# Optimization experiments

Hardware: AMD Instinct MI355X
Metric: run time of the kernel (lower is better)

## Reference

```python
import jax, jax.numpy as jnp
import numpy as np

# (dv=3, dc=6)-regular Tanner graph: M checks, N=2M vars, E=M*dc edges
M, N, DV, DC, D, B, T = 1024, 2048, 3, 6, 8, 128, 5
CIN = DC * D          # check-MLP in/out dim = 48
VIN = DV * D + 1      # var-MLP in/out dim  = 25 (extra scalar = LLR)
HC, HV = 4 * CIN, 4 * VIN
EPS = 1e-6


def _graph():
    # variable j connects to checks (j + l) % M, l = 0..DV-1 -> every check has degree DC
    var_nbrs = (np.arange(N)[:, None] + np.arange(DV)[None, :]) % M   # [N, DV] check ids
    # var-edge id e = j*DV + l ; sort edges by check to get check-slot ordering
    order = np.argsort(var_nbrs.reshape(-1), kind='stable')           # check-edge p -> var-edge e
    chk_nbrs = (order // DV).reshape(M, DC)                           # var id in each check slot
    inv_order = np.argsort(order)                                     # var-edge e -> check-edge p
    return chk_nbrs, order, inv_order


def setup_inputs() -> dict:
    key = jax.random.key(0)
    ks = jax.random.split(key, 12)
    chk_nbrs, order, inv_order = _graph()
    prior = np.clip(np.random.default_rng(0).uniform(0.005, 0.05, size=N), EPS, 1 - EPS)
    prior_llr = jnp.asarray(np.log((1.0 - prior) / prior), jnp.float32)

    def lin_w(k, g, nin, nout):
        return jax.random.normal(k, (g, nin, nout), jnp.float32) / np.sqrt(nin)

    def lin_b(k, g, nout):
        return 0.02 * jax.random.normal(k, (g, nout), jnp.float32)

    return {
        "syndromes": jax.random.randint(ks[0], (B, M), 0, 2, jnp.int32),
        "prior_llr": prior_llr,
        "chk_w1": lin_w(ks[1], M, CIN, HC), "chk_b1": lin_b(ks[2], M, HC),
        "chk_w2": lin_w(ks[3], M, HC, CIN), "chk_b2": lin_b(ks[4], M, CIN),
        "var_w1": lin_w(ks[5], N, VIN, HV), "var_b1": lin_b(ks[6], N, HV),
        "var_w2": lin_w(ks[7], N, HV, VIN), "var_b2": lin_b(ks[8], N, VIN),
        "chk_nbrs": jnp.asarray(chk_nbrs, jnp.int32),      # [M, DC] var id per check slot
        "c2v_gather": jnp.asarray(inv_order, jnp.int32),   # var-edge -> check-edge perm
        "v2c_gather": jnp.asarray(order, jnp.int32),       # check-edge -> var-edge perm
    }


def reference(syndromes, prior_llr, chk_w1, chk_b1, chk_w2, chk_b2,
              var_w1, var_b1, var_w2, var_b2, chk_nbrs, c2v_gather, v2c_gather):
    synd_sgn = (1 - 2 * syndromes).astype(jnp.float32)                    # [B, M]
    prior_b = jnp.broadcast_to(prior_llr, (B, N))[..., None]              # [B, N, 1]

    def chk_mlp(x):  # x: [B, M, CIN], per-check grouped GEMM
        h = jax.nn.gelu(jnp.einsum('bmi,mih->bmh', x, chk_w1) + chk_b1, approximate=False)
        return jnp.einsum('bmh,mho->bmo', h, chk_w2) + chk_b2

    def var_mlp(x):  # x: [B, N, VIN]
        h = jax.nn.gelu(jnp.einsum('bni,nih->bnh', x, var_w1) + var_b1, approximate=False)
        return jnp.einsum('bnh,nho->bno', h, var_w2) + var_b2

    # init check in-messages: zeros with first component = prior LLR of neighbor var
    chk_in = jnp.zeros((B, M, DC, D), jnp.float32).at[..., 0].set(prior_llr[chk_nbrs][None])

    def step(chk_in, _):
        y = chk_mlp(chk_in.reshape(B, M, CIN)).reshape(B, M, DC, D)
        y = y * synd_sgn[:, :, None, None]                                # syndrome sign flip
        var_in = y.reshape(B, M * DC, D)[:, c2v_gather]                   # scatter c->v as gather
        x = jnp.concatenate([var_in.reshape(B, N, DV * D), prior_b], axis=-1)
        out = var_mlp(x)
        llr = out[..., DV * D]                                            # [B, N]
        msg = out[..., :DV * D].reshape(B, N * DV, D)
        chk_in_new = msg[:, v2c_gather].reshape(B, M, DC, D)              # scatter v->c as gather
        return chk_in_new, llr

    _, llrs = jax.lax.scan(step, chk_in, None, length=T)
    return llrs  # [T, B, N]
```

## Files before the change

kernel.cpp:

```cpp
#include <hip/hip_runtime.h>
#include <math.h>

#define MM 1024
#define NN 2048
#define BB 128
#define TT 5
#define EE 6144

typedef __bf16 bf16x8 __attribute__((ext_vector_type(8)));
typedef float  f32x4  __attribute__((ext_vector_type(4)));
typedef unsigned int u32x4 __attribute__((ext_vector_type(4)));

__device__ __forceinline__ float gelu_fast(float x) {
    float xe = x * 0.70710678118654752f;
    float ax = fabsf(xe);
    float t  = __builtin_amdgcn_rcpf(1.0f + 0.3275911f * ax);
    float p  = t * (0.254829592f + t * (-0.284496736f + t * (1.421413741f +
               t * (-1.453152027f + t * 1.061405429f))));
    float er = 1.0f - p * __expf(-xe * xe);
    er = copysignf(er, xe);
    return 0.5f * x * (1.0f + er);
}

__device__ __forceinline__ void wave_lds_fence() {
    asm volatile("s_waitcnt lgkmcnt(0)" ::: "memory");
}

__global__ __launch_bounds__(256)
void init_kernel(const float* __restrict__ prior, __bf16* __restrict__ v2c)
{
    int idx = blockIdx.x * 256 + threadIdx.x;
    int e = idx >> 7;
    bf16x8 v;
    #pragma unroll
    for (int j = 0; j < 8; ++j) v[j] = (__bf16)0.0f;
    v[0] = (__bf16)prior[e / 3];
    *(bf16x8*)(v2c + (size_t)idx * 8) = v;
}

__global__ __launch_bounds__(256)
void prep_chk(const float* __restrict__ w1g, const float* __restrict__ w2g,
              __bf16* __restrict__ wchk)
{
    const int m = blockIdx.x;
    const int tid = threadIdx.x, w = tid >> 6, l = tid & 63, qq = l >> 4, cc = l & 15;
    const float* s1 = w1g + (size_t)m * (48 * 192);
    const float* s2 = w2g + (size_t)m * (192 * 48);
    __bf16* dst = wchk + (size_t)m * 21504;
    for (int f = w; f < 42; f += 4) {
        bf16x8 v;
        if (f < 24) {
            int kt = f / 12, nt = f % 12;
            #pragma unroll
            for (int j = 0; j < 8; ++j) {
                int k = kt * 32 + qq * 8 + j, n = nt * 16 + cc;
                v[j] = (k < 48) ? (__bf16)s1[k * 192 + n] : (__bf16)0.0f;
            }
        } else {
            int g = f - 24, kt = g / 3, nt = g % 3;
            #pragma unroll
            for (int j = 0; j < 8; ++j) {
                int k = kt * 32 + qq * 8 + j, n = nt * 16 + cc;
                v[j] = (__bf16)s2[k * 48 + n];
            }
        }
        *(bf16x8*)(dst + f * 512 + l * 8) = v;
    }
}

__global__ __launch_bounds__(256)
void prep_var(const float* __restrict__ w1g, const float* __restrict__ w2g,
              __bf16* __restrict__ wvar)
{
    const int nv = blockIdx.x;
    const int tid = threadIdx.x, w = tid >> 6, l = tid & 63, qq = l >> 4, cc = l & 15;
    const float* s1 = w1g + (size_t)nv * (25 * 100);
    const float* s2 = w2g + (size_t)nv * (100 * 25);
    __bf16* dst = wvar + (size_t)nv * 7680;
    for (int f = w; f < 15; f += 4) {
        bf16x8 v;
        if (f < 7) {
            int nt = f;
            #pragma unroll
            for (int j = 0; j < 8; ++j) {
                int k = qq * 8 + j, n = nt * 16 + cc;
                v[j] = (k < 25 && n < 100) ? (__bf16)s1[k * 100 + n] : (__bf16)0.0f;
            }
        } else {
            int g = f - 7, kt = g >> 1, nt = g & 1;
            #pragma unroll
            for (int j = 0; j < 8; ++j) {
                int k = kt * 32 + qq * 8 + j, n = nt * 16 + cc;
                v[j] = (k < 100 && n < 25) ? (__bf16)s2[k * 25 + n] : (__bf16)0.0f;
            }
        }
        *(bf16x8*)(dst + f * 512 + l * 8) = v;
    }
}

__global__ __launch_bounds__(256, 2)
void chk_kernel(const __bf16* __restrict__ wchk,
                const float* __restrict__ b1g, const float* __restrict__ b2g,
                const int* __restrict__ syndromes,
                const int* __restrict__ v2c_gather,
                const __bf16* __restrict__ v2c, __bf16* __restrict__ c2v)
{
    const int m = blockIdx.x;
    const int tid = threadIdx.x;
    const int w = tid >> 6, l = tid & 63, q = l >> 4, c = l & 15;

    __shared__ __align__(16) __bf16 wAll[42 * 512];
    __shared__ __align__(16) __bf16 hb[4 * 3200];
    __shared__ float b1s[192];
    __shared__ float b2s[48];
    __shared__ float sgns[128];
    __shared__ int   eg[6];

    {
        const __bf16* wsrc = wchk + (size_t)m * 21504;
        for (int f = w; f < 42; f += 4) {
            u32x4 v = *(const u32x4*)(wsrc + f * 512 + l * 8);
            *(u32x4*)(wAll + f * 512 + l * 8) = v;
        }
    }
    if (tid < 192) b1s[tid] = b1g[(size_t)m * 192 + tid];
    if (tid < 48)  b2s[tid] = b2g[(size_t)m * 48 + tid];
    if (tid < 128) sgns[tid] = (float)(1 - 2 * syndromes[(size_t)tid * MM + m]);
    if (tid < 6)   eg[tid] = v2c_gather[m * 6 + tid];
    __syncthreads();

    const __bf16* w1f = wAll;
    const __bf16* w2f = wAll + 24 * 512;
    __bf16* myh = hb + w * 3200;
    const int e0 = eg[q];
    const int e1 = (q < 2) ? eg[4 + q] : 0;

    for (int t2 = 0; t2 < 2; ++t2) {
        const int bt = t2 * 64 + w * 16;

        bf16x8 a0 = *(const bf16x8*)(v2c + ((size_t)e0 * BB + bt + c) * 8);
        bf16x8 a1;
        #pragma unroll
        for (int j = 0; j < 8; ++j) a1[j] = (__bf16)0.0f;
        if (q < 2) a1 = *(const bf16x8*)(v2c + ((size_t)e1 * BB + bt + c) * 8);

        f32x4 acc[12];
        #pragma unroll
        for (int nt = 0; nt < 12; ++nt) {
            bf16x8 bf0 = *(const bf16x8*)(w1f + (nt * 64 + l) * 8);
            bf16x8 bf1 = *(const bf16x8*)(w1f + ((12 + nt) * 64 + l) * 8);
            f32x4 z = {0.f, 0.f, 0.f, 0.f};
            z = __builtin_amdgcn_mfma_f32_16x16x32_bf16(a0, bf0, z, 0, 0, 0);
            z = __builtin_amdgcn_mfma_f32_16x16x32_bf16(a1, bf1, z, 0, 0, 0);
            acc[nt] = z;
        }

        #pragma unroll
        for (int nt = 0; nt < 12; ++nt) {
            #pragma unroll
            for (int r = 0; r < 4; ++r) {
                int row = q * 4 + r, col = nt * 16 + c;
                float h = acc[nt][r] + b1s[col];
                myh[row * 200 + col] = (__bf16)gelu_fast(h);
            }
        }
        wave_lds_fence();

        f32x4 acc2[3];
        #pragma unroll
        for (int nt = 0; nt < 3; ++nt) acc2[nt] = (f32x4){0.f, 0.f, 0.f, 0.f};
        #pragma unroll
        for (int kt = 0; kt < 6; ++kt) {
            bf16x8 a = *(const bf16x8*)(myh + c * 200 + kt * 32 + q * 8);
            #pragma unroll
            for (int nt = 0; nt < 3; ++nt) {
                bf16x8 bfr = *(const bf16x8*)(w2f + ((kt * 3 + nt) * 64 + l) * 8);
                acc2[nt] = __builtin_amdgcn_mfma_f32_16x16x32_bf16(a, bfr, acc2[nt], 0, 0, 0);
            }
        }
        wave_lds_fence();

        #pragma unroll
        for (int nt = 0; nt < 3; ++nt) {
            #pragma unroll
            for (int r = 0; r < 4; ++r) {
                int row = q * 4 + r, col = nt * 16 + c;
                float yv = (acc2[nt][r] + b2s[col]) * sgns[bt + row];
                myh[row * 72 + col] = (__bf16)yv;
            }
        }
        wave_lds_fence();

        {
            int s = l >> 4, row = l & 15;
            u32x4 vv = *(const u32x4*)(myh + row * 72 + s * 8);
            *(u32x4*)(c2v + ((size_t)(m * 6 + s) * BB + bt + row) * 8) = vv;
            if (l < 32) {
                int s2 = (64 + l) >> 4, row2 = l & 15;
                u32x4 v2 = *(const u32x4*)(myh + row2 * 72 + s2 * 8);
                *(u32x4*)(c2v + ((size_t)(m * 6 + s2) * BB + bt + row2) * 8) = v2;
            }
        }
        wave_lds_fence();
    }
}

__global__ __launch_bounds__(256, 4)
void var_kernel(const __bf16* __restrict__ wvar,
                const float* __restrict__ b1g, const float* __restrict__ b2g,
                const int* __restrict__ c2v_gather, const float* __restrict__ prior,
                const __bf16* __restrict__ c2v, __bf16* __restrict__ v2c,
                float* __restrict__ llr_out)
{
    const int nv = blockIdx.x;
    const int tid = threadIdx.x;
    const int w = tid >> 6, l = tid & 63, q = l >> 4, c = l & 15;

    __shared__ __align__(16) __bf16 wAll[15 * 512];
    __shared__ __align__(16) __bf16 hb[4 * 2816];
    __shared__ float b1s[112];
    __shared__ float b2s[32];
    __shared__ int   cgs[3];

    {
        u32x4* zp = (u32x4*)hb;
        for (int i = tid; i < 1408; i += 256) zp[i] = (u32x4){0, 0, 0, 0};
    }
    {
        const __bf16* wsrc = wvar + (size_t)nv * 7680;
        for (int f = w; f < 15; f += 4) {
            u32x4 v = *(const u32x4*)(wsrc + f * 512 + l * 8);
            *(u32x4*)(wAll + f * 512 + l * 8) = v;
        }
    }
    if (tid < 112) b1s[tid] = (tid < 100) ? b1g[(size_t)nv * 100 + tid] : 0.0f;
    if (tid < 32)  b2s[tid] = (tid < 25) ? b2g[(size_t)nv * 25 + tid] : 0.0f;
    if (tid < 3)   cgs[tid] = c2v_gather[nv * 3 + tid];
    __syncthreads();

    const __bf16* w1vf = wAll;
    const __bf16* w2vf = wAll + 7 * 512;
    __bf16* myh = hb + w * 2816;
    __bf16* myy = hb + w * 2816 + 2176;
    const float pr = prior[nv];
    const __bf16 prbf = (__bf16)pr;
    const int ep = (q < 3) ? cgs[q] : 0;

    for (int t2 = 0; t2 < 2; ++t2) {
        const int bt = t2 * 64 + w * 16;

        bf16x8 a;
        #pragma unroll
        for (int j = 0; j < 8; ++j) a[j] = (__bf16)0.0f;
        if (q < 3) {
            a = *(const bf16x8*)(c2v + ((size_t)ep * BB + bt + c) * 8);
        } else {
            a[0] = prbf;
        }

        f32x4 acc[7];
        #pragma unroll
        for (int nt = 0; nt < 7; ++nt) {
            bf16x8 bfr = *(const bf16x8*)(w1vf + (nt * 64 + l) * 8);
            f32x4 z = {0.f, 0.f, 0.f, 0.f};
            acc[nt] = __builtin_amdgcn_mfma_f32_16x16x32_bf16(a, bfr, z, 0, 0, 0);
        }

        #pragma unroll
        for (int nt = 0; nt < 7; ++nt) {
            #pragma unroll
            for (int r = 0; r < 4; ++r) {
                int row = q * 4 + r, col = nt * 16 + c;
                float h = acc[nt][r] + b1s[col];
                myh[row * 136 + col] = (__bf16)gelu_fast(h);
            }
        }
        wave_lds_fence();

        f32x4 acc2[2];
        acc2[0] = (f32x4){0.f, 0.f, 0.f, 0.f};
        acc2[1] = (f32x4){0.f, 0.f, 0.f, 0.f};
        #pragma unroll
        for (int kt = 0; kt < 4; ++kt) {
            bf16x8 a2 = *(const bf16x8*)(myh + c * 136 + kt * 32 + q * 8);
            #pragma unroll
            for (int nt = 0; nt < 2; ++nt) {
                bf16x8 bfr = *(const bf16x8*)(w2vf + ((kt * 2 + nt) * 64 + l) * 8);
                acc2[nt] = __builtin_amdgcn_mfma_f32_16x16x32_bf16(a2, bfr, acc2[nt], 0, 0, 0);
            }
        }
        wave_lds_fence();

        #pragma unroll
        for (int nt = 0; nt < 2; ++nt) {
            #pragma unroll
            for (int r = 0; r < 4; ++r) {
                int row = q * 4 + r, col = nt * 16 + c;
                float yv = acc2[nt][r] + b2s[col];
                if (col < 24) myy[row * 40 + col] = (__bf16)yv;
                else if (col == 24) llr_out[(size_t)(bt + row) * NN + nv] = yv;
            }
        }
        wave_lds_fence();

        if (l < 48) {
            int s = l >> 4, row = l & 15;
            u32x4 vv = *(const u32x4*)(myy + row * 40 + s * 8);
            *(u32x4*)(v2c + ((size_t)(nv * 3 + s) * BB + bt + row) * 8) = vv;
        }
        wave_lds_fence();
    }
}

extern "C" void kernel_launch(void* const* d_in, const int* in_sizes, int n_in,
                              void* d_out, int out_size, void* d_ws, size_t ws_size,
                              hipStream_t stream) {
    const int*   syndromes = (const int*)  d_in[0];
    const float* prior_llr = (const float*)d_in[1];
    const float* chk_w1    = (const float*)d_in[2];
    const float* chk_b1    = (const float*)d_in[3];
    const float* chk_w2    = (const float*)d_in[4];
    const float* chk_b2    = (const float*)d_in[5];
    const float* var_w1    = (const float*)d_in[6];
    const float* var_b1    = (const float*)d_in[7];
    const float* var_w2    = (const float*)d_in[8];
    const float* var_b2    = (const float*)d_in[9];
    const int*   c2v_g     = (const int*)  d_in[11];
    const int*   v2c_g     = (const int*)  d_in[12];

    float* out = (float*)d_out;

    __bf16* v2c  = (__bf16*)d_ws;
    __bf16* c2v  = v2c + (size_t)EE * BB * 8;
    __bf16* wchk = c2v + (size_t)EE * BB * 8;
    __bf16* wvar = wchk + (size_t)MM * 21504;

    prep_chk<<<MM, 256, 0, stream>>>(chk_w1, chk_w2, wchk);
    prep_var<<<NN, 256, 0, stream>>>(var_w1, var_w2, wvar);
    init_kernel<<<EE * BB / 256, 256, 0, stream>>>(prior_llr, v2c);

    for (int t = 0; t < TT; ++t) {
        chk_kernel<<<MM, 256, 0, stream>>>(wchk, chk_b1, chk_b2,
                                           syndromes, v2c_g, v2c, c2v);
        var_kernel<<<NN, 256, 0, stream>>>(wvar, var_b1, var_b2,
                                           c2v_g, prior_llr, c2v, v2c,
                                           out + (size_t)t * BB * NN);
    }
}
```

Before: 475.2 us.

## Read MLP weights directly from global memory, merge prep kernels, skip final message write

The check and var kernels no longer stage per-node weights, biases, signs and gather indices through LDS behind a block barrier. Each wave now reads the MFMA weight fragments straight from global memory and keeps biases and syndrome signs in registers, which cuts LDS use and lets chk_kernel target 4 blocks per SM. The two weight-prep kernels are merged into one launch with one wave per fragment, and the last var pass skips writing v2c messages that are never read. In exchange, all four waves of a block re-read the same weights from global memory or cache instead of sharing an LDS copy.

```diff
diff --git a/kernel.cpp b/kernel.cpp
--- a/kernel.cpp
+++ b/kernel.cpp
@@ -10,6 +10,7 @@
 typedef __bf16 bf16x8 __attribute__((ext_vector_type(8)));
 typedef float  f32x4  __attribute__((ext_vector_type(4)));
 typedef unsigned int u32x4 __attribute__((ext_vector_type(4)));
+typedef unsigned int u32x2 __attribute__((ext_vector_type(2)));
 
 __device__ __forceinline__ float gelu_fast(float x) {
     float xe = x * 0.70710678118654752f;
@@ -39,66 +40,59 @@
 }
 
 __global__ __launch_bounds__(256)
-void prep_chk(const float* __restrict__ w1g, const float* __restrict__ w2g,
-              __bf16* __restrict__ wchk)
+void prep_all(const float* __restrict__ cw1, const float* __restrict__ cw2,
+              const float* __restrict__ vw1, const float* __restrict__ vw2,
+              __bf16* __restrict__ wchk, __bf16* __restrict__ wvar)
 {
-    const int m = blockIdx.x;
-    const int tid = threadIdx.x, w = tid >> 6, l = tid & 63, qq = l >> 4, cc = l & 15;
-    const float* s1 = w1g + (size_t)m * (48 * 192);
-    const float* s2 = w2g + (size_t)m * (192 * 48);
-    __bf16* dst = wchk + (size_t)m * 21504;
-    for (int f = w; f < 42; f += 4) {
-        bf16x8 v;
+    const int wid = blockIdx.x * 4 + (threadIdx.x >> 6);
+    const int l = threadIdx.x & 63, qq = l >> 4, cc = l & 15;
+    bf16x8 v;
+    __bf16* dst;
+    if (wid < MM * 42) {
+        const int m = wid / 42, f = wid % 42;
         if (f < 24) {
-            int kt = f / 12, nt = f % 12;
+            const int kt = f / 12, nt = f % 12;
+            const float* s1 = cw1 + (size_t)m * (48 * 192);
             #pragma unroll
             for (int j = 0; j < 8; ++j) {
-                int k = kt * 32 + qq * 8 + j, n = nt * 16 + cc;
-                v[j] = (k < 48) ? (__bf16)s1[k * 192 + n] : (__bf16)0.0f;
+                int k = kt * 32 + qq * 8 + j;
+                v[j] = (k < 48) ? (__bf16)s1[k * 192 + nt * 16 + cc] : (__bf16)0.0f;
             }
         } else {
-            int g = f - 24, kt = g / 3, nt = g % 3;
+            const int g = f - 24, kt = g / 3, nt = g % 3;
+            const float* s2 = cw2 + (size_t)m * (192 * 48);
             #pragma unroll
             for (int j = 0; j < 8; ++j) {
-                int k = kt * 32 + qq * 8 + j, n = nt * 16 + cc;
-                v[j] = (__bf16)s2[k * 48 + n];
-            }
-        }
-        *(bf16x8*)(dst + f * 512 + l * 8) = v;
-    }
-}
-
-__global__ __launch_bounds__(256)
-void prep_var(const float* __restrict__ w1g, const float* __restrict__ w2g,
-              __bf16* __restrict__ wvar)
-{
-    const int nv = blockIdx.x;
-    const int tid = threadIdx.x, w = tid >> 6, l = tid & 63, qq = l >> 4, cc = l & 15;
-    const float* s1 = w1g + (size_t)nv * (25 * 100);
-    const float* s2 = w2g + (size_t)nv * (100 * 25);
-    __bf16* dst = wvar + (size_t)nv * 7680;
-    for (int f = w; f < 15; f += 4) {
-        bf16x8 v;
+                int k = kt * 32 + qq * 8 + j;
+                v[j] = (__bf16)s2[k * 48 + nt * 16 + cc];
+            }
+        }
+        dst = wchk + (size_t)m * 21504 + (f * 64 + l) * 8;
+    } else {
+        const int tsk = wid - MM * 42;
+        const int nv = tsk / 15, f = tsk % 15;
         if (f < 7) {
-            int nt = f;
+            const float* s1 = vw1 + (size_t)nv * (25 * 100);
             #pragma unroll
             for (int j = 0; j < 8; ++j) {
-                int k = qq * 8 + j, n = nt * 16 + cc;
+                int k = qq * 8 + j, n = f * 16 + cc;
                 v[j] = (k < 25 && n < 100) ? (__bf16)s1[k * 100 + n] : (__bf16)0.0f;
             }
         } else {
-            int g = f - 7, kt = g >> 1, nt = g & 1;
+            const int g = f - 7, kt = g >> 1, nt = g & 1;
+            const float* s2 = vw2 + (size_t)nv * (100 * 25);
             #pragma unroll
             for (int j = 0; j < 8; ++j) {
                 int k = kt * 32 + qq * 8 + j, n = nt * 16 + cc;
                 v[j] = (k < 100 && n < 25) ? (__bf16)s2[k * 25 + n] : (__bf16)0.0f;
             }
         }
-        *(bf16x8*)(dst + f * 512 + l * 8) = v;
-    }
-}
-
-__global__ __launch_bounds__(256, 2)
+        dst = wvar + (size_t)nv * 7680 + (f * 64 + l) * 8;
+    }
+    *(bf16x8*)dst = v;
+}
+
+__global__ __launch_bounds__(256, 4)
 void chk_kernel(const __bf16* __restrict__ wchk,
                 const float* __restrict__ b1g, const float* __restrict__ b2g,
                 const int* __restrict__ syndromes,
@@ -109,31 +103,26 @@
     const int tid = threadIdx.x;
     const int w = tid >> 6, l = tid & 63, q = l >> 4, c = l & 15;
 
-    __shared__ __align__(16) __bf16 wAll[42 * 512];
     __shared__ __align__(16) __bf16 hb[4 * 3200];
-    __shared__ float b1s[192];
-    __shared__ float b2s[48];
-    __shared__ float sgns[128];
-    __shared__ int   eg[6];
-
-    {
-        const __bf16* wsrc = wchk + (size_t)m * 21504;
-        for (int f = w; f < 42; f += 4) {
-            u32x4 v = *(const u32x4*)(wsrc + f * 512 + l * 8);
-            *(u32x4*)(wAll + f * 512 + l * 8) = v;
-        }
-    }
-    if (tid < 192) b1s[tid] = b1g[(size_t)m * 192 + tid];
-    if (tid < 48)  b2s[tid] = b2g[(size_t)m * 48 + tid];
-    if (tid < 128) sgns[tid] = (float)(1 - 2 * syndromes[(size_t)tid * MM + m]);
-    if (tid < 6)   eg[tid] = v2c_gather[m * 6 + tid];
-    __syncthreads();
-
-    const __bf16* w1f = wAll;
-    const __bf16* w2f = wAll + 24 * 512;
     __bf16* myh = hb + w * 3200;
-    const int e0 = eg[q];
-    const int e1 = (q < 2) ? eg[4 + q] : 0;
+
+    const __bf16* wb = wchk + (size_t)m * 21504;
+
+    float b1v[12], b2v[3], sg[8];
+    #pragma unroll
+    for (int nt = 0; nt < 12; ++nt) b1v[nt] = b1g[(size_t)m * 192 + nt * 16 + c];
+    #pragma unroll
+    for (int nt = 0; nt < 3; ++nt)  b2v[nt] = b2g[(size_t)m * 48 + nt * 16 + c];
+    #pragma unroll
+    for (int t2 = 0; t2 < 2; ++t2)
+        #pragma unroll
+        for (int r = 0; r < 4; ++r) {
+            int row = t2 * 64 + w * 16 + q * 4 + r;
+            sg[t2 * 4 + r] = (float)(1 - 2 * syndromes[(size_t)row * MM + m]);
+        }
+
+    const int e0 = v2c_gather[m * 6 + q];
+    const int e1 = (q < 2) ? v2c_gather[m * 6 + 4 + q] : 0;
 
     for (int t2 = 0; t2 < 2; ++t2) {
         const int bt = t2 * 64 + w * 16;
@@ -147,8 +136,8 @@
         f32x4 acc[12];
         #pragma unroll
         for (int nt = 0; nt < 12; ++nt) {
-            bf16x8 bf0 = *(const bf16x8*)(w1f + (nt * 64 + l) * 8);
-            bf16x8 bf1 = *(const bf16x8*)(w1f + ((12 + nt) * 64 + l) * 8);
+            bf16x8 bf0 = *(const bf16x8*)(wb + (nt * 64 + l) * 8);
+            bf16x8 bf1 = *(const bf16x8*)(wb + ((12 + nt) * 64 + l) * 8);
             f32x4 z = {0.f, 0.f, 0.f, 0.f};
             z = __builtin_amdgcn_mfma_f32_16x16x32_bf16(a0, bf0, z, 0, 0, 0);
             z = __builtin_amdgcn_mfma_f32_16x16x32_bf16(a1, bf1, z, 0, 0, 0);
@@ -159,9 +148,8 @@
         for (int nt = 0; nt < 12; ++nt) {
             #pragma unroll
             for (int r = 0; r < 4; ++r) {
-                int row = q * 4 + r, col = nt * 16 + c;
-                float h = acc[nt][r] + b1s[col];
-                myh[row * 200 + col] = (__bf16)gelu_fast(h);
+                int row = q * 4 + r;
+                myh[row * 200 + nt * 16 + c] = (__bf16)gelu_fast(acc[nt][r] + b1v[nt]);
             }
         }
         wave_lds_fence();
@@ -174,7 +162,7 @@
             bf16x8 a = *(const bf16x8*)(myh + c * 200 + kt * 32 + q * 8);
             #pragma unroll
             for (int nt = 0; nt < 3; ++nt) {
-                bf16x8 bfr = *(const bf16x8*)(w2f + ((kt * 3 + nt) * 64 + l) * 8);
+                bf16x8 bfr = *(const bf16x8*)(wb + ((24 + kt * 3 + nt) * 64 + l) * 8);
                 acc2[nt] = __builtin_amdgcn_mfma_f32_16x16x32_bf16(a, bfr, acc2[nt], 0, 0, 0);
             }
         }
@@ -184,9 +172,8 @@
         for (int nt = 0; nt < 3; ++nt) {
             #pragma unroll
             for (int r = 0; r < 4; ++r) {
-                int row = q * 4 + r, col = nt * 16 + c;
-                float yv = (acc2[nt][r] + b2s[col]) * sgns[bt + row];
-                myh[row * 72 + col] = (__bf16)yv;
+                int row = q * 4 + r;
+                myh[row * 72 + nt * 16 + c] = (__bf16)((acc2[nt][r] + b2v[nt]) * sg[t2 * 4 + r]);
             }
         }
         wave_lds_fence();
@@ -196,7 +183,7 @@
             u32x4 vv = *(const u32x4*)(myh + row * 72 + s * 8);
             *(u32x4*)(c2v + ((size_t)(m * 6 + s) * BB + bt + row) * 8) = vv;
             if (l < 32) {
-                int s2 = (64 + l) >> 4, row2 = l & 15;
+                int s2 = 4 + (l >> 4), row2 = l & 15;
                 u32x4 v2 = *(const u32x4*)(myh + row2 * 72 + s2 * 8);
                 *(u32x4*)(c2v + ((size_t)(m * 6 + s2) * BB + bt + row2) * 8) = v2;
             }
@@ -210,41 +197,36 @@
                 const float* __restrict__ b1g, const float* __restrict__ b2g,
                 const int* __restrict__ c2v_gather, const float* __restrict__ prior,
                 const __bf16* __restrict__ c2v, __bf16* __restrict__ v2c,
-                float* __restrict__ llr_out)
+                float* __restrict__ llr_out, int last)
 {
     const int nv = blockIdx.x;
     const int tid = threadIdx.x;
     const int w = tid >> 6, l = tid & 63, q = l >> 4, c = l & 15;
 
-    __shared__ __align__(16) __bf16 wAll[15 * 512];
     __shared__ __align__(16) __bf16 hb[4 * 2816];
-    __shared__ float b1s[112];
-    __shared__ float b2s[32];
-    __shared__ int   cgs[3];
+    __bf16* myh = hb + w * 2816;
+    __bf16* myy = myh + 2176;
+
+    const __bf16* wb = wvar + (size_t)nv * 7680;
 
     {
-        u32x4* zp = (u32x4*)hb;
-        for (int i = tid; i < 1408; i += 256) zp[i] = (u32x4){0, 0, 0, 0};
-    }
-    {
-        const __bf16* wsrc = wvar + (size_t)nv * 7680;
-        for (int f = w; f < 15; f += 4) {
-            u32x4 v = *(const u32x4*)(wsrc + f * 512 + l * 8);
-            *(u32x4*)(wAll + f * 512 + l * 8) = v;
-        }
-    }
-    if (tid < 112) b1s[tid] = (tid < 100) ? b1g[(size_t)nv * 100 + tid] : 0.0f;
-    if (tid < 32)  b2s[tid] = (tid < 25) ? b2g[(size_t)nv * 25 + tid] : 0.0f;
-    if (tid < 3)   cgs[tid] = c2v_gather[nv * 3 + tid];
-    __syncthreads();
-
-    const __bf16* w1vf = wAll;
-    const __bf16* w2vf = wAll + 7 * 512;
-    __bf16* myh = hb + w * 2816;
-    __bf16* myy = hb + w * 2816 + 2176;
-    const float pr = prior[nv];
-    const __bf16 prbf = (__bf16)pr;
-    const int ep = (q < 3) ? cgs[q] : 0;
+        int r = l >> 2, g = l & 3;
+        *(u32x2*)(myh + r * 136 + 112 + g * 4) = (u32x2){0, 0};
+    }
+
+    float b1v[7], b2v[2];
+    #pragma unroll
+    for (int nt = 0; nt < 7; ++nt) {
+        int col = nt * 16 + c;
+        b1v[nt] = (col < 100) ? b1g[(size_t)nv * 100 + col] : 0.0f;
+    }
+    #pragma unroll
+    for (int nt = 0; nt < 2; ++nt) {
+        int col = nt * 16 + c;
+        b2v[nt] = (col < 25) ? b2g[(size_t)nv * 25 + col] : 0.0f;
+    }
+    const __bf16 prbf = (__bf16)prior[nv];
+    const int ep = (q < 3) ? c2v_gather[nv * 3 + q] : 0;
 
     for (int t2 = 0; t2 < 2; ++t2) {
         const int bt = t2 * 64 + w * 16;
@@ -252,16 +234,13 @@
         bf16x8 a;
         #pragma unroll
         for (int j = 0; j < 8; ++j) a[j] = (__bf16)0.0f;
-        if (q < 3) {
-            a = *(const bf16x8*)(c2v + ((size_t)ep * BB + bt + c) * 8);
-        } else {
-            a[0] = prbf;
-        }
+        if (q < 3) a = *(const bf16x8*)(c2v + ((size_t)ep * BB + bt + c) * 8);
+        else       a[0] = prbf;
 
         f32x4 acc[7];
         #pragma unroll
         for (int nt = 0; nt < 7; ++nt) {
-            bf16x8 bfr = *(const bf16x8*)(w1vf + (nt * 64 + l) * 8);
+            bf16x8 bfr = *(const bf16x8*)(wb + (nt * 64 + l) * 8);
             f32x4 z = {0.f, 0.f, 0.f, 0.f};
             acc[nt] = __builtin_amdgcn_mfma_f32_16x16x32_bf16(a, bfr, z, 0, 0, 0);
         }
@@ -270,9 +249,8 @@
         for (int nt = 0; nt < 7; ++nt) {
             #pragma unroll
             for (int r = 0; r < 4; ++r) {
-                int row = q * 4 + r, col = nt * 16 + c;
-                float h = acc[nt][r] + b1s[col];
-                myh[row * 136 + col] = (__bf16)gelu_fast(h);
+                int row = q * 4 + r;
+                myh[row * 136 + nt * 16 + c] = (__bf16)gelu_fast(acc[nt][r] + b1v[nt]);
             }
         }
         wave_lds_fence();
@@ -285,7 +263,7 @@
             bf16x8 a2 = *(const bf16x8*)(myh + c * 136 + kt * 32 + q * 8);
             #pragma unroll
             for (int nt = 0; nt < 2; ++nt) {
-                bf16x8 bfr = *(const bf16x8*)(w2vf + ((kt * 2 + nt) * 64 + l) * 8);
+                bf16x8 bfr = *(const bf16x8*)(wb + ((7 + kt * 2 + nt) * 64 + l) * 8);
                 acc2[nt] = __builtin_amdgcn_mfma_f32_16x16x32_bf16(a2, bfr, acc2[nt], 0, 0, 0);
             }
         }
@@ -296,14 +274,14 @@
             #pragma unroll
             for (int r = 0; r < 4; ++r) {
                 int row = q * 4 + r, col = nt * 16 + c;
-                float yv = acc2[nt][r] + b2s[col];
+                float yv = acc2[nt][r] + b2v[nt];
                 if (col < 24) myy[row * 40 + col] = (__bf16)yv;
                 else if (col == 24) llr_out[(size_t)(bt + row) * NN + nv] = yv;
             }
         }
         wave_lds_fence();
 
-        if (l < 48) {
+        if (!last && l < 48) {
             int s = l >> 4, row = l & 15;
             u32x4 vv = *(const u32x4*)(myy + row * 40 + s * 8);
             *(u32x4*)(v2c + ((size_t)(nv * 3 + s) * BB + bt + row) * 8) = vv;
@@ -335,8 +313,9 @@
     __bf16* wchk = c2v + (size_t)EE * BB * 8;
     __bf16* wvar = wchk + (size_t)MM * 21504;
 
-    prep_chk<<<MM, 256, 0, stream>>>(chk_w1, chk_w2, wchk);
-    prep_var<<<NN, 256, 0, stream>>>(var_w1, var_w2, wvar);
+    prep_all<<<(MM * 42 + NN * 15) / 4, 256, 0, stream>>>(chk_w1, chk_w2,
+                                                          var_w1, var_w2,
+                                                          wchk, wvar);
     init_kernel<<<EE * BB / 256, 256, 0, stream>>>(prior_llr, v2c);
 
     for (int t = 0; t < TT; ++t) {
@@ -344,6 +323,7 @@
                                            syndromes, v2c_g, v2c, c2v);
         var_kernel<<<NN, 256, 0, stream>>>(wvar, var_b1, var_b2,
                                            c2v_g, prior_llr, c2v, v2c,
-                                           out + (size_t)t * BB * NN);
-    }
-}
+                                           out + (size_t)t * BB * NN,
+                                           (t == TT - 1) ? 1 : 0);
+    }
+}
```

Result: faster. 443.8 us (-6.6%).
